# Kernel optimization log

Hardware: AMD Instinct MI355X
Metric: run time of the kernel (lower is better)

## Reference

```python
import jax, jax.numpy as jnp
import numpy as np

N_EMBD = 1024
N_HEAD = 16

def setup_inputs() -> dict:
    key = jax.random.key(0)
    ks = jax.random.split(key, 8)
    C = N_EMBD
    s = 1.0 / np.sqrt(C)
    return {
        "x": jax.random.normal(ks[0], (8, 1024, C), jnp.float32),
        "encoder_output": jax.random.normal(ks[1], (8, 576, C), jnp.float32),
        "Wq": jax.random.normal(ks[2], (C, C), jnp.float32) * s,      # torch Linear weight [out,in]
        "bq": jnp.zeros((C,), jnp.float32),
        "Wkv": jax.random.normal(ks[3], (2 * C, C), jnp.float32) * s,
        "bkv": jnp.zeros((2 * C,), jnp.float32),
        "Wo": jax.random.normal(ks[4], (C, C), jnp.float32) * s,
        "bo": jnp.zeros((C,), jnp.float32),
    }

def reference(x, encoder_output, Wq, bq, Wkv, bkv, Wo, bo):
    B, T, C = x.shape
    I = encoder_output.shape[1]
    H, D = N_HEAD, C // N_HEAD
    q = jnp.einsum('btc,oc->bto', x, Wq) + bq                     # [B,T,C]
    kv = jnp.einsum('bic,oc->bio', encoder_output, Wkv) + bkv     # [B,I,2C]
    k, v = kv[..., :C], kv[..., C:]
    q = q.reshape(B, T, H, D).transpose(0, 2, 1, 3)               # [B,H,T,D]
    k = k.reshape(B, I, H, D).transpose(0, 2, 1, 3)               # [B,H,I,D]
    v = v.reshape(B, I, H, D).transpose(0, 2, 1, 3)               # [B,H,I,D]
    att = jnp.einsum('bhtd,bhid->bhti', q, k) * (1.0 / np.sqrt(D))
    att = jax.nn.softmax(att, axis=-1)                            # no mask: buffer unused in fwd
    y = jnp.einsum('bhti,bhid->bhtd', att, v)
    y = y.transpose(0, 2, 1, 3).reshape(B, T, C)
    return jnp.einsum('btc,oc->bto', y, Wo) + bo
```

## Files before the change

kernel.cpp:

```cpp
#include <hip/hip_runtime.h>
#include <type_traits>

typedef __bf16 bf16_t;
typedef __bf16 bfx8 __attribute__((ext_vector_type(8)));
typedef float  fx4  __attribute__((ext_vector_type(4)));

#define MFMA_BF16 __builtin_amdgcn_mfma_f32_16x16x32_bf16

#define BB 8
#define TT 1024
#define II 576
#define HH 16
#define DD 64
#define CC 1024

__device__ __forceinline__ void load_lds16(const void* g, void* l) {
    __builtin_amdgcn_global_load_lds(
        (const __attribute__((address_space(1))) void*)g,
        (__attribute__((address_space(3))) void*)l, 16, 0, 0);
}

__global__ __launch_bounds__(256)
void cvt_all(const float* __restrict__ x,  const float* __restrict__ enc,
             const float* __restrict__ wq, const float* __restrict__ wkv,
             const float* __restrict__ wo, const float* __restrict__ bq,
             const float* __restrict__ bkv,const float* __restrict__ bo,
             bf16_t* __restrict__ xb,  bf16_t* __restrict__ encb,
             bf16_t* __restrict__ wqb, bf16_t* __restrict__ wkvb,
             bf16_t* __restrict__ wob, bf16_t* __restrict__ bqb,
             bf16_t* __restrict__ bkvb,bf16_t* __restrict__ bob)
{
    const long total = 17305600;
    for (long e = ((long)blockIdx.x * 256 + threadIdx.x) * 8; e < total;
         e += (long)gridDim.x * 256 * 8) {
        const float* s; bf16_t* d; long off; float sc = 1.0f;
        if      (e <  8388608) { s = x;   d = xb;   off = e; }
        else if (e < 13107200) { s = enc; d = encb; off = e -  8388608; }
        else if (e < 14155776) { s = wq;  d = wqb;  off = e - 13107200; sc = 0.125f; }
        else if (e < 16252928) { s = wkv; d = wkvb; off = e - 14155776; }
        else if (e < 17301504) { s = wo;  d = wob;  off = e - 16252928; }
        else if (e < 17302528) { s = bq;  d = bqb;  off = e - 17301504; sc = 0.125f; }
        else if (e < 17304576) { s = bkv; d = bkvb; off = e - 17302528; }
        else                   { s = bo;  d = bob;  off = e - 17304576; }
        fx4 a = *reinterpret_cast<const fx4*>(s + off);
        fx4 b = *reinterpret_cast<const fx4*>(s + off + 4);
        bfx8 v;
#pragma unroll
        for (int i = 0; i < 4; i++) {
            v[i]     = (bf16_t)(a[i] * sc);
            v[4 + i] = (bf16_t)(b[i] * sc);
        }
        *reinterpret_cast<bfx8*>(d + off) = v;
    }
}

template<typename TOUT>
__global__ __launch_bounds__(256)
void gemm_lds(const bf16_t* __restrict__ A, const bf16_t* __restrict__ W,
              const bf16_t* __restrict__ bias, TOUT* __restrict__ out,
              int M, int N, int K)
{
    __shared__ __align__(16) bf16_t As[128 * 64];
    __shared__ __align__(16) bf16_t Bs[128 * 64];

    const int tid  = threadIdx.x;
    const int lane = tid & 63;
    const int w    = tid >> 6;
    const int wm   = (w >> 1) * 64;
    const int wn   = (w & 1) * 64;
    const int m0   = blockIdx.y * 128;
    const int n0   = blockIdx.x * 128;
    const int lrow = lane & 15;
    const int quad = lane >> 4;

    fx4 acc[4][4];
#pragma unroll
    for (int i = 0; i < 4; i++)
#pragma unroll
        for (int j = 0; j < 4; j++) acc[i][j] = (fx4)0.0f;

    for (int k0 = 0; k0 < K; k0 += 64) {
        __syncthreads();
#pragma unroll
        for (int j = 0; j < 4; j++) {
            int e0  = (w * 4 + j) * 512;
            int e   = e0 + lane * 8;
            int row = e >> 6;
            int col = e & 63;
            load_lds16(&A[(long)(m0 + row) * K + k0 + col], &As[e0]);
            load_lds16(&W[(long)(n0 + row) * K + k0 + col], &Bs[e0]);
        }
        __syncthreads();

#pragma unroll
        for (int kk = 0; kk < 2; kk++) {
            bfx8 af[4], bfr[4];
#pragma unroll
            for (int i = 0; i < 4; i++)
                af[i] = *reinterpret_cast<const bfx8*>(
                    &As[(wm + i * 16 + lrow) * 64 + kk * 32 + quad * 8]);
#pragma unroll
            for (int j = 0; j < 4; j++)
                bfr[j] = *reinterpret_cast<const bfx8*>(
                    &Bs[(wn + j * 16 + lrow) * 64 + kk * 32 + quad * 8]);
#pragma unroll
            for (int i = 0; i < 4; i++)
#pragma unroll
                for (int j = 0; j < 4; j++)
                    acc[i][j] = MFMA_BF16(af[i], bfr[j], acc[i][j], 0, 0, 0);
        }
    }

#pragma unroll
    for (int i = 0; i < 4; i++) {
#pragma unroll
        for (int j = 0; j < 4; j++) {
            int col  = n0 + wn + j * 16 + lrow;
            float bv = (float)bias[col];
            int row0 = m0 + wm + i * 16 + quad * 4;
#pragma unroll
            for (int r = 0; r < 4; r++)
                out[(long)(row0 + r) * N + col] = (TOUT)(acc[i][j][r] + bv);
        }
    }
}

template<typename TA, typename TOUT>
__global__ __launch_bounds__(256)
void gemm_bt_bias(const TA* __restrict__ A, const float* __restrict__ W,
                  const float* __restrict__ bias, TOUT* __restrict__ out,
                  int M, int N, int K, float escale)
{
    __shared__ __align__(16) bf16_t As[128][40];
    __shared__ __align__(16) bf16_t Bs[128][40];

    const int tid  = threadIdx.x;
    const int lane = tid & 63;
    const int wave = tid >> 6;
    const int wm   = (wave >> 1) * 64;
    const int wn   = (wave & 1) * 64;
    const int m0   = blockIdx.y * 128;
    const int n0   = blockIdx.x * 128;
    const int lrow = lane & 15;
    const int quad = lane >> 4;

    fx4 acc[4][4];
#pragma unroll
    for (int i = 0; i < 4; i++)
#pragma unroll
        for (int j = 0; j < 4; j++) acc[i][j] = (fx4)0.0f;

    for (int k0 = 0; k0 < K; k0 += 32) {
        __syncthreads();
#pragma unroll
        for (int r = 0; r < 2; ++r) {
            int idx = tid + r * 256;
            int row = idx >> 2;
            int col = (idx & 3) * 8;

            bfx8 av;
            if constexpr (std::is_same<TA, float>::value) {
                const float* sa = &A[(long)(m0 + row) * K + k0 + col];
                fx4 a0 = *reinterpret_cast<const fx4*>(sa);
                fx4 a1 = *reinterpret_cast<const fx4*>(sa + 4);
#pragma unroll
                for (int e = 0; e < 4; e++) {
                    av[e]     = (bf16_t)a0[e];
                    av[4 + e] = (bf16_t)a1[e];
                }
            } else {
                av = *reinterpret_cast<const bfx8*>(&A[(long)(m0 + row) * K + k0 + col]);
            }
            *reinterpret_cast<bfx8*>(&As[row][col]) = av;

            const float* sw = &W[(long)(n0 + row) * K + k0 + col];
            fx4 b0 = *reinterpret_cast<const fx4*>(sw);
            fx4 b1 = *reinterpret_cast<const fx4*>(sw + 4);
            bfx8 bv;
#pragma unroll
            for (int e = 0; e < 4; e++) {
                bv[e]     = (bf16_t)b0[e];
                bv[4 + e] = (bf16_t)b1[e];
            }
            *reinterpret_cast<bfx8*>(&Bs[row][col]) = bv;
        }
        __syncthreads();

        bfx8 af[4], bfr[4];
#pragma unroll
        for (int i = 0; i < 4; i++)
            af[i] = *reinterpret_cast<const bfx8*>(&As[wm + i * 16 + lrow][quad * 8]);
#pragma unroll
        for (int j = 0; j < 4; j++)
            bfr[j] = *reinterpret_cast<const bfx8*>(&Bs[wn + j * 16 + lrow][quad * 8]);
#pragma unroll
        for (int i = 0; i < 4; i++)
#pragma unroll
            for (int j = 0; j < 4; j++)
                acc[i][j] = MFMA_BF16(af[i], bfr[j], acc[i][j], 0, 0, 0);
    }

#pragma unroll
    for (int i = 0; i < 4; i++) {
#pragma unroll
        for (int j = 0; j < 4; j++) {
            int col  = n0 + wn + j * 16 + lrow;
            float bv = bias[col];
            int row0 = m0 + wm + i * 16 + quad * 4;
#pragma unroll
            for (int r = 0; r < 4; r++)
                out[(long)(row0 + r) * N + col] = (TOUT)((acc[i][j][r] + bv) * escale);
        }
    }
}

__global__ __launch_bounds__(256)
void attn_kernel(const bf16_t* __restrict__ q, const bf16_t* __restrict__ kv,
                 bf16_t* __restrict__ y, int b0)
{
    __shared__ __align__(16) bf16_t Ks[64][72];
    __shared__ __align__(16) bf16_t Vt[64][72];
    __shared__ __align__(16) bf16_t Ps[4][16][72];

    const int tid  = threadIdx.x;
    const int lane = tid & 63;
    const int w    = tid >> 6;
    const int lrow = lane & 15;
    const int quad = lane >> 4;
    const int bl = blockIdx.z;
    const int b  = b0 + bl;
    const int h  = blockIdx.y;
    const int t0 = blockIdx.x * 64;

    const int trow = t0 + w * 16 + lrow;
    bfx8 qf[2];
#pragma unroll
    for (int ks = 0; ks < 2; ++ks)
        qf[ks] = *reinterpret_cast<const bfx8*>(
            &q[(long)(b * TT + trow) * CC + h * 64 + ks * 32 + quad * 8]);

    float mrow[4], lsum[4];
    fx4 o[4];
#pragma unroll
    for (int r = 0; r < 4; r++) { mrow[r] = -1e30f; lsum[r] = 0.f; }
#pragma unroll
    for (int dt = 0; dt < 4; dt++) o[dt] = (fx4)0.0f;

    const int srow = tid >> 2;
    const int scol = (tid & 3) * 16;

    for (int ic = 0; ic < II / 64; ++ic) {
        __syncthreads();
        {
            long base = (long)(bl * II + ic * 64 + srow) * 2048 + h * 64 + scol;
            bfx8 k0v = *reinterpret_cast<const bfx8*>(&kv[base]);
            bfx8 k1v = *reinterpret_cast<const bfx8*>(&kv[base + 8]);
            *reinterpret_cast<bfx8*>(&Ks[srow][scol])     = k0v;
            *reinterpret_cast<bfx8*>(&Ks[srow][scol + 8]) = k1v;
            bfx8 v0 = *reinterpret_cast<const bfx8*>(&kv[base + 1024]);
            bfx8 v1 = *reinterpret_cast<const bfx8*>(&kv[base + 1032]);
#pragma unroll
            for (int e = 0; e < 8; e++) {
                Vt[scol + e][srow]     = v0[e];
                Vt[scol + 8 + e][srow] = v1[e];
            }
        }
        __syncthreads();

        fx4 s[4];
#pragma unroll
        for (int nt = 0; nt < 4; nt++) {
            s[nt] = (fx4)0.0f;
#pragma unroll
            for (int ks = 0; ks < 2; ks++) {
                bfx8 bf = *reinterpret_cast<const bfx8*>(
                    &Ks[nt * 16 + lrow][ks * 32 + quad * 8]);
                s[nt] = MFMA_BF16(qf[ks], bf, s[nt], 0, 0, 0);
            }
        }

        float p[4][4];
#pragma unroll
        for (int r = 0; r < 4; r++) {
            float mx = -1e30f;
#pragma unroll
            for (int nt = 0; nt < 4; nt++) mx = fmaxf(mx, s[nt][r]);
#pragma unroll
            for (int off = 1; off < 16; off <<= 1)
                mx = fmaxf(mx, __shfl_xor(mx, off, 64));
            float mnew  = fmaxf(mrow[r], mx);
            float alpha = __expf(mrow[r] - mnew);
            mrow[r] = mnew;
            float ps = 0.f;
#pragma unroll
            for (int nt = 0; nt < 4; nt++) {
                float pv = __expf(s[nt][r] - mnew);
                p[nt][r] = pv;
                ps += pv;
            }
#pragma unroll
            for (int off = 1; off < 16; off <<= 1)
                ps += __shfl_xor(ps, off, 64);
            lsum[r] = lsum[r] * alpha + ps;
#pragma unroll
            for (int dt = 0; dt < 4; dt++) o[dt][r] *= alpha;
        }

#pragma unroll
        for (int nt = 0; nt < 4; nt++)
#pragma unroll
            for (int r = 0; r < 4; r++)
                Ps[w][quad * 4 + r][nt * 16 + lrow] = (bf16_t)p[nt][r];

        __asm__ __volatile__("s_waitcnt lgkmcnt(0)" ::: "memory");

#pragma unroll
        for (int dt = 0; dt < 4; dt++) {
#pragma unroll
            for (int ks = 0; ks < 2; ks++) {
                bfx8 af = *reinterpret_cast<const bfx8*>(
                    &Ps[w][lrow][ks * 32 + quad * 8]);
                bfx8 bf = *reinterpret_cast<const bfx8*>(
                    &Vt[dt * 16 + lrow][ks * 32 + quad * 8]);
                o[dt] = MFMA_BF16(af, bf, o[dt], 0, 0, 0);
            }
        }
    }

#pragma unroll
    for (int dt = 0; dt < 4; dt++) {
#pragma unroll
        for (int r = 0; r < 4; r++) {
            int t = t0 + w * 16 + quad * 4 + r;
            y[(long)(b * TT + t) * CC + h * 64 + dt * 16 + lrow] =
                (bf16_t)(o[dt][r] / lsum[r]);
        }
    }
}

extern "C" void kernel_launch(void* const* d_in, const int* in_sizes, int n_in,
                              void* d_out, int out_size, void* d_ws, size_t ws_size,
                              hipStream_t stream)
{
    const float* x   = (const float*)d_in[0];
    const float* enc = (const float*)d_in[1];
    const float* Wq  = (const float*)d_in[2];
    const float* bq  = (const float*)d_in[3];
    const float* Wkv = (const float*)d_in[4];
    const float* bkv = (const float*)d_in[5];
    const float* Wo  = (const float*)d_in[6];
    const float* bo  = (const float*)d_in[7];
    float* out = (float*)d_out;

    bf16_t* qbuf = (bf16_t*)d_out;

    const size_t primary_need = 35520512ULL * 2;

    if (ws_size >= primary_need) {
        bf16_t* kvbuf = (bf16_t*)d_ws;
        bf16_t* ybuf  = kvbuf + (size_t)9437184;
        bf16_t* xb    = ybuf  + (size_t)8388608;
        bf16_t* encb  = xb    + (size_t)8388608;
        bf16_t* Wqb   = encb  + (size_t)4718592;
        bf16_t* Wkvb  = Wqb   + (size_t)1048576;
        bf16_t* Wob   = Wkvb  + (size_t)2097152;
        bf16_t* bqb   = Wob   + (size_t)1048576;
        bf16_t* bkvb  = bqb   + 1024;
        bf16_t* bob   = bkvb  + 2048;

        cvt_all<<<4096, 256, 0, stream>>>(x, enc, Wq, Wkv, Wo, bq, bkv, bo,
                                          xb, encb, Wqb, Wkvb, Wob, bqb, bkvb, bob);

        gemm_lds<bf16_t><<<dim3(8, 64), 256, 0, stream>>>(
            xb, Wqb, bqb, qbuf, 8192, 1024, 1024);
        gemm_lds<bf16_t><<<dim3(16, 36), 256, 0, stream>>>(
            encb, Wkvb, bkvb, kvbuf, 4608, 2048, 1024);
        attn_kernel<<<dim3(16, 16, 8), 256, 0, stream>>>(qbuf, kvbuf, ybuf, 0);
        gemm_lds<float><<<dim3(8, 64), 256, 0, stream>>>(
            ybuf, Wob, bob, out, 8192, 1024, 1024);
    } else {
        bf16_t* kvbuf = (bf16_t*)d_ws;
        gemm_bt_bias<float, bf16_t><<<dim3(8, 64), 256, 0, stream>>>(
            x, Wq, bq, qbuf, 8192, 1024, 1024, 0.125f);

        const size_t full_need = ((size_t)4608 * 2048 + (size_t)8192 * 1024) * 2;
        if (ws_size >= full_need) {
            bf16_t* ybuf = kvbuf + (size_t)4608 * 2048;
            gemm_bt_bias<float, bf16_t><<<dim3(16, 36), 256, 0, stream>>>(
                enc, Wkv, bkv, kvbuf, 4608, 2048, 1024, 1.0f);
            attn_kernel<<<dim3(16, 16, 8), 256, 0, stream>>>(qbuf, kvbuf, ybuf, 0);
            gemm_bt_bias<bf16_t, float><<<dim3(8, 64), 256, 0, stream>>>(
                ybuf, Wo, bo, out, 8192, 1024, 1024, 1.0f);
        } else {
            bf16_t* ybuf = kvbuf + (size_t)1152 * 2048;
            for (int b0 = 0; b0 < BB; b0 += 2) {
                gemm_bt_bias<float, bf16_t><<<dim3(16, 9), 256, 0, stream>>>(
                    enc + (size_t)b0 * II * CC, Wkv, bkv, kvbuf, 1152, 2048, 1024, 1.0f);
                attn_kernel<<<dim3(16, 16, 2), 256, 0, stream>>>(qbuf, kvbuf, ybuf, b0);
            }
            gemm_bt_bias<bf16_t, float><<<dim3(8, 64), 256, 0, stream>>>(
                ybuf, Wo, bo, out, 8192, 1024, 1024, 1.0f);
        }
    }
}
```

Measured before the change: 297.7 us.

## Fuse Q and KV projections, swizzle LDS, pre-layout K/V^T for attention

Merges the Q and KV projection GEMMs into one launch and shrinks the GEMM tile to 128x64 so more blocks are in flight. An XOR swizzle on the LDS column index is meant to cut bank conflicts. The KV epilogue writes K as head-major and V already transposed, so attention can load tiles with plain vector copies. The new attention kernel gives each wave 32 query rows to reuse K/V tiles, and drops the max subtraction from the softmax. The cost is strided, uncoalesced scatter stores in the KV epilogue and an unguarded exp that could overflow on larger scores.

```diff
diff --git a/kernel.cpp b/kernel.cpp
--- a/kernel.cpp
+++ b/kernel.cpp
@@ -54,67 +54,183 @@
     }
 }
 
-template<typename TOUT>
+
+#define GEMM_STAGE(A_, W_, K_)                                                \
+    {                                                                         \
+        _Pragma("unroll")                                                     \
+        for (int j = 0; j < 4; j++) {                                         \
+            int e0  = (w * 4 + j) * 512;                                      \
+            int row = (e0 >> 6) + (lane >> 3);                                \
+            load_lds16(&A_[(long)(m0 + row) * K_ + k0 + colsw], &As[e0]);     \
+        }                                                                     \
+        _Pragma("unroll")                                                     \
+        for (int j = 0; j < 2; j++) {                                         \
+            int e0  = (w * 2 + j) * 512;                                      \
+            int row = (e0 >> 6) + (lane >> 3);                                \
+            load_lds16(&W_[(long)(n0 + row) * K_ + k0 + colsw], &Bs[e0]);     \
+        }                                                                     \
+    }
+
+#define GEMM_MFMA()                                                           \
+    _Pragma("unroll")                                                         \
+    for (int kk = 0; kk < 2; kk++) {                                          \
+        bfx8 af[4], bfr[2];                                                   \
+        _Pragma("unroll")                                                     \
+        for (int i = 0; i < 4; i++) {                                         \
+            int R = wm + i * 16 + lrow;                                       \
+            af[i] = *reinterpret_cast<const bfx8*>(                           \
+                &As[R * 64 + (((kk * 4 + quad) ^ (lrow & 7)) * 8)]);          \
+        }                                                                     \
+        _Pragma("unroll")                                                     \
+        for (int j = 0; j < 2; j++) {                                         \
+            int R = wn + j * 16 + lrow;                                       \
+            bfr[j] = *reinterpret_cast<const bfx8*>(                          \
+                &Bs[R * 64 + (((kk * 4 + quad) ^ (lrow & 7)) * 8)]);          \
+        }                                                                     \
+        _Pragma("unroll")                                                     \
+        for (int i = 0; i < 4; i++)                                           \
+            _Pragma("unroll")                                                 \
+            for (int j = 0; j < 2; j++)                                       \
+                acc[i][j] = MFMA_BF16(af[i], bfr[j], acc[i][j], 0, 0, 0);     \
+    }
+
 __global__ __launch_bounds__(256)
-void gemm_lds(const bf16_t* __restrict__ A, const bf16_t* __restrict__ W,
-              const bf16_t* __restrict__ bias, TOUT* __restrict__ out,
-              int M, int N, int K)
+void gemm_qkv(const bf16_t* __restrict__ xb,  const bf16_t* __restrict__ Wqb,
+              const bf16_t* __restrict__ bqb, bf16_t* __restrict__ qout,
+              const bf16_t* __restrict__ encb,const bf16_t* __restrict__ Wkvb,
+              const bf16_t* __restrict__ bkvb,
+              bf16_t* __restrict__ Kbuf, bf16_t* __restrict__ VTbuf)
 {
     __shared__ __align__(16) bf16_t As[128 * 64];
-    __shared__ __align__(16) bf16_t Bs[128 * 64];
+    __shared__ __align__(16) bf16_t Bs[64 * 64];
 
     const int tid  = threadIdx.x;
     const int lane = tid & 63;
     const int w    = tid >> 6;
     const int wm   = (w >> 1) * 64;
-    const int wn   = (w & 1) * 64;
-    const int m0   = blockIdx.y * 128;
-    const int n0   = blockIdx.x * 128;
+    const int wn   = (w & 1) * 32;
     const int lrow = lane & 15;
     const int quad = lane >> 4;
-
-    fx4 acc[4][4];
+    const int colsw = (((lane & 7) ^ ((lane >> 3) & 7)) * 8);
+
+    int bid = blockIdx.x;
+    const bf16_t *A, *W, *bias;
+    int m0, n0, mode;
+    if (bid < 1024) {
+        mode = 0; A = xb; W = Wqb; bias = bqb;
+        m0 = (bid >> 4) * 128; n0 = (bid & 15) * 64;
+    } else {
+        bid -= 1024;
+        mode = 1; A = encb; W = Wkvb; bias = bkvb;
+        m0 = (bid >> 5) * 128; n0 = (bid & 31) * 64;
+    }
+    const int K = 1024;
+
+    fx4 acc[4][2];
 #pragma unroll
     for (int i = 0; i < 4; i++)
 #pragma unroll
-        for (int j = 0; j < 4; j++) acc[i][j] = (fx4)0.0f;
+        for (int j = 0; j < 2; j++) acc[i][j] = (fx4)0.0f;
 
     for (int k0 = 0; k0 < K; k0 += 64) {
         __syncthreads();
-#pragma unroll
-        for (int j = 0; j < 4; j++) {
-            int e0  = (w * 4 + j) * 512;
-            int e   = e0 + lane * 8;
-            int row = e >> 6;
-            int col = e & 63;
-            load_lds16(&A[(long)(m0 + row) * K + k0 + col], &As[e0]);
-            load_lds16(&W[(long)(n0 + row) * K + k0 + col], &Bs[e0]);
-        }
-        __syncthreads();
-
-#pragma unroll
-        for (int kk = 0; kk < 2; kk++) {
-            bfx8 af[4], bfr[4];
-#pragma unroll
-            for (int i = 0; i < 4; i++)
-                af[i] = *reinterpret_cast<const bfx8*>(
-                    &As[(wm + i * 16 + lrow) * 64 + kk * 32 + quad * 8]);
-#pragma unroll
-            for (int j = 0; j < 4; j++)
-                bfr[j] = *reinterpret_cast<const bfx8*>(
-                    &Bs[(wn + j * 16 + lrow) * 64 + kk * 32 + quad * 8]);
-#pragma unroll
-            for (int i = 0; i < 4; i++)
-#pragma unroll
-                for (int j = 0; j < 4; j++)
-                    acc[i][j] = MFMA_BF16(af[i], bfr[j], acc[i][j], 0, 0, 0);
-        }
-    }
-
-#pragma unroll
-    for (int i = 0; i < 4; i++) {
-#pragma unroll
-        for (int j = 0; j < 4; j++) {
+        GEMM_STAGE(A, W, K)
+        __syncthreads();
+        GEMM_MFMA()
+    }
+
+    if (mode == 0) {
+#pragma unroll
+        for (int i = 0; i < 4; i++)
+#pragma unroll
+            for (int j = 0; j < 2; j++) {
+                int col  = n0 + wn + j * 16 + lrow;
+                float bv = (float)bias[col];
+                int row0 = m0 + wm + i * 16 + quad * 4;
+#pragma unroll
+                for (int r = 0; r < 4; r++)
+                    qout[(long)(row0 + r) * 1024 + col] =
+                        (bf16_t)(acc[i][j][r] + bv);
+            }
+    } else if (n0 < 1024) {
+#pragma unroll
+        for (int i = 0; i < 4; i++) {
+            int row0 = m0 + wm + i * 16 + quad * 4;
+#pragma unroll
+            for (int r = 0; r < 4; r++) {
+                unsigned m = row0 + r;
+                unsigned b = m / 576u;
+                unsigned ii = m - b * 576u;
+#pragma unroll
+                for (int j = 0; j < 2; j++) {
+                    int col = n0 + wn + j * 16 + lrow;
+                    int h = col >> 6, d = col & 63;
+                    Kbuf[(((long)(b * 16 + h) * 576 + ii) << 6) + d] =
+                        (bf16_t)(acc[i][j][r] + (float)bias[col]);
+                }
+            }
+        }
+    } else {
+#pragma unroll
+        for (int i = 0; i < 4; i++) {
+            int row0 = m0 + wm + i * 16 + quad * 4;
+#pragma unroll
+            for (int r = 0; r < 4; r++) {
+                unsigned m = row0 + r;
+                unsigned b = m / 576u;
+                unsigned ii = m - b * 576u;
+#pragma unroll
+                for (int j = 0; j < 2; j++) {
+                    int col = n0 + wn + j * 16 + lrow;
+                    int c2 = col - 1024;
+                    int h = c2 >> 6, d = c2 & 63;
+                    VTbuf[((long)(b * 16 + h) * 64 + d) * 576 + ii] =
+                        (bf16_t)(acc[i][j][r] + (float)bias[col]);
+                }
+            }
+        }
+    }
+}
+
+template<typename TOUT>
+__global__ __launch_bounds__(256)
+void gemm2(const bf16_t* __restrict__ A, const bf16_t* __restrict__ W,
+           const bf16_t* __restrict__ bias, TOUT* __restrict__ out,
+           int M, int N, int K)
+{
+    __shared__ __align__(16) bf16_t As[128 * 64];
+    __shared__ __align__(16) bf16_t Bs[64 * 64];
+
+    const int tid  = threadIdx.x;
+    const int lane = tid & 63;
+    const int w    = tid >> 6;
+    const int wm   = (w >> 1) * 64;
+    const int wn   = (w & 1) * 32;
+    const int lrow = lane & 15;
+    const int quad = lane >> 4;
+    const int colsw = (((lane & 7) ^ ((lane >> 3) & 7)) * 8);
+
+    const int ntiles = N >> 6;
+    const int m0 = (blockIdx.x / ntiles) * 128;
+    const int n0 = (blockIdx.x % ntiles) * 64;
+
+    fx4 acc[4][2];
+#pragma unroll
+    for (int i = 0; i < 4; i++)
+#pragma unroll
+        for (int j = 0; j < 2; j++) acc[i][j] = (fx4)0.0f;
+
+    for (int k0 = 0; k0 < K; k0 += 64) {
+        __syncthreads();
+        GEMM_STAGE(A, W, K)
+        __syncthreads();
+        GEMM_MFMA()
+    }
+
+#pragma unroll
+    for (int i = 0; i < 4; i++)
+#pragma unroll
+        for (int j = 0; j < 2; j++) {
             int col  = n0 + wn + j * 16 + lrow;
             float bv = (float)bias[col];
             int row0 = m0 + wm + i * 16 + quad * 4;
@@ -122,7 +238,117 @@
             for (int r = 0; r < 4; r++)
                 out[(long)(row0 + r) * N + col] = (TOUT)(acc[i][j][r] + bv);
         }
-    }
+}
+
+__global__ __launch_bounds__(256)
+void attn2(const bf16_t* __restrict__ q, const bf16_t* __restrict__ Kbuf,
+           const bf16_t* __restrict__ VTbuf, bf16_t* __restrict__ y)
+{
+    __shared__ __align__(16) bf16_t Ks[64][72];
+    __shared__ __align__(16) bf16_t Vt[64][72];
+    __shared__ __align__(16) bf16_t Ps[4][32][72];
+
+    const int tid  = threadIdx.x;
+    const int lane = tid & 63;
+    const int w    = tid >> 6;
+    const int lrow = lane & 15;
+    const int quad = lane >> 4;
+    const int b  = blockIdx.z;
+    const int h  = blockIdx.y;
+    const int t0 = blockIdx.x * 128;
+
+    const bf16_t* kb = Kbuf  + ((long)(b * 16 + h) * 576) * 64;
+    const bf16_t* vb = VTbuf + ((long)(b * 16 + h) * 64) * 576;
+
+    bfx8 qf[2][2];
+#pragma unroll
+    for (int mt = 0; mt < 2; mt++)
+#pragma unroll
+        for (int ks = 0; ks < 2; ks++)
+            qf[mt][ks] = *reinterpret_cast<const bfx8*>(
+                &q[(long)(b * TT + t0 + w * 32 + mt * 16 + lrow) * CC +
+                   h * 64 + ks * 32 + quad * 8]);
+
+    fx4 o[2][4];
+    float lsum[2][4];
+#pragma unroll
+    for (int mt = 0; mt < 2; mt++)
+#pragma unroll
+        for (int dt = 0; dt < 4; dt++) o[mt][dt] = (fx4)0.0f;
+#pragma unroll
+    for (int mt = 0; mt < 2; mt++)
+#pragma unroll
+        for (int r = 0; r < 4; r++) lsum[mt][r] = 0.f;
+
+    const int srow = tid >> 3;
+    const int scol = (tid & 7) * 8;
+
+    for (int ic = 0; ic < II / 64; ++ic) {
+        __syncthreads();
+#pragma unroll
+        for (int it = 0; it < 2; it++) {
+            int rr = srow + it * 32;
+            *reinterpret_cast<bfx8*>(&Ks[rr][scol]) =
+                *reinterpret_cast<const bfx8*>(&kb[(long)(ic * 64 + rr) * 64 + scol]);
+            *reinterpret_cast<bfx8*>(&Vt[rr][scol]) =
+                *reinterpret_cast<const bfx8*>(&vb[(long)rr * 576 + ic * 64 + scol]);
+        }
+        __syncthreads();
+
+#pragma unroll
+        for (int mt = 0; mt < 2; mt++) {
+            fx4 s[4];
+#pragma unroll
+            for (int nt = 0; nt < 4; nt++) {
+                s[nt] = (fx4)0.0f;
+#pragma unroll
+                for (int ks = 0; ks < 2; ks++) {
+                    bfx8 bfr = *reinterpret_cast<const bfx8*>(
+                        &Ks[nt * 16 + lrow][ks * 32 + quad * 8]);
+                    s[nt] = MFMA_BF16(qf[mt][ks], bfr, s[nt], 0, 0, 0);
+                }
+            }
+#pragma unroll
+            for (int nt = 0; nt < 4; nt++)
+#pragma unroll
+                for (int r = 0; r < 4; r++) {
+                    float p = __expf(s[nt][r]);
+                    lsum[mt][r] += p;
+                    Ps[w][mt * 16 + quad * 4 + r][nt * 16 + lrow] = (bf16_t)p;
+                }
+        }
+
+        __asm__ __volatile__("s_waitcnt lgkmcnt(0)" ::: "memory");
+
+#pragma unroll
+        for (int mt = 0; mt < 2; mt++)
+#pragma unroll
+            for (int dt = 0; dt < 4; dt++)
+#pragma unroll
+                for (int ks = 0; ks < 2; ks++) {
+                    bfx8 af = *reinterpret_cast<const bfx8*>(
+                        &Ps[w][mt * 16 + lrow][ks * 32 + quad * 8]);
+                    bfx8 bfr = *reinterpret_cast<const bfx8*>(
+                        &Vt[dt * 16 + lrow][ks * 32 + quad * 8]);
+                    o[mt][dt] = MFMA_BF16(af, bfr, o[mt][dt], 0, 0, 0);
+                }
+    }
+
+#pragma unroll
+    for (int mt = 0; mt < 2; mt++)
+#pragma unroll
+        for (int r = 0; r < 4; r++) {
+            float l = lsum[mt][r];
+#pragma unroll
+            for (int off = 1; off < 16; off <<= 1)
+                l += __shfl_xor(l, off, 64);
+            float inv = 1.0f / l;
+            int t = t0 + w * 32 + mt * 16 + quad * 4 + r;
+#pragma unroll
+            for (int dt = 0; dt < 4; dt++)
+                y[(long)(b * TT + t) * CC + h * 64 + dt * 16 + lrow] =
+                    (bf16_t)(o[mt][dt][r] * inv);
+        }
 }
 
 template<typename TA, typename TOUT>
@@ -157,31 +383,23 @@
             int idx = tid + r * 256;
             int row = idx >> 2;
             int col = (idx & 3) * 8;
-
             bfx8 av;
             if constexpr (std::is_same<TA, float>::value) {
                 const float* sa = &A[(long)(m0 + row) * K + k0 + col];
                 fx4 a0 = *reinterpret_cast<const fx4*>(sa);
                 fx4 a1 = *reinterpret_cast<const fx4*>(sa + 4);
 #pragma unroll
-                for (int e = 0; e < 4; e++) {
-                    av[e]     = (bf16_t)a0[e];
-                    av[4 + e] = (bf16_t)a1[e];
-                }
+                for (int e = 0; e < 4; e++) { av[e] = (bf16_t)a0[e]; av[4+e] = (bf16_t)a1[e]; }
             } else {
                 av = *reinterpret_cast<const bfx8*>(&A[(long)(m0 + row) * K + k0 + col]);
             }
             *reinterpret_cast<bfx8*>(&As[row][col]) = av;
-
             const float* sw = &W[(long)(n0 + row) * K + k0 + col];
             fx4 b0 = *reinterpret_cast<const fx4*>(sw);
             fx4 b1 = *reinterpret_cast<const fx4*>(sw + 4);
             bfx8 bv;
 #pragma unroll
-            for (int e = 0; e < 4; e++) {
-                bv[e]     = (bf16_t)b0[e];
-                bv[4 + e] = (bf16_t)b1[e];
-            }
+            for (int e = 0; e < 4; e++) { bv[e] = (bf16_t)b0[e]; bv[4+e] = (bf16_t)b1[e]; }
             *reinterpret_cast<bfx8*>(&Bs[row][col]) = bv;
         }
         __syncthreads();
@@ -201,7 +419,7 @@
     }
 
 #pragma unroll
-    for (int i = 0; i < 4; i++) {
+    for (int i = 0; i < 4; i++)
 #pragma unroll
         for (int j = 0; j < 4; j++) {
             int col  = n0 + wn + j * 16 + lrow;
@@ -211,7 +429,6 @@
             for (int r = 0; r < 4; r++)
                 out[(long)(row0 + r) * N + col] = (TOUT)((acc[i][j][r] + bv) * escale);
         }
-    }
 }
 
 __global__ __launch_bounds__(256)
@@ -273,9 +490,9 @@
             s[nt] = (fx4)0.0f;
 #pragma unroll
             for (int ks = 0; ks < 2; ks++) {
-                bfx8 bf = *reinterpret_cast<const bfx8*>(
+                bfx8 bfr = *reinterpret_cast<const bfx8*>(
                     &Ks[nt * 16 + lrow][ks * 32 + quad * 8]);
-                s[nt] = MFMA_BF16(qf[ks], bf, s[nt], 0, 0, 0);
+                s[nt] = MFMA_BF16(qf[ks], bfr, s[nt], 0, 0, 0);
             }
         }
 
@@ -315,27 +532,25 @@
         __asm__ __volatile__("s_waitcnt lgkmcnt(0)" ::: "memory");
 
 #pragma unroll
-        for (int dt = 0; dt < 4; dt++) {
+        for (int dt = 0; dt < 4; dt++)
 #pragma unroll
             for (int ks = 0; ks < 2; ks++) {
                 bfx8 af = *reinterpret_cast<const bfx8*>(
                     &Ps[w][lrow][ks * 32 + quad * 8]);
-                bfx8 bf = *reinterpret_cast<const bfx8*>(
+                bfx8 bfr = *reinterpret_cast<const bfx8*>(
                     &Vt[dt * 16 + lrow][ks * 32 + quad * 8]);
-                o[dt] = MFMA_BF16(af, bf, o[dt], 0, 0, 0);
-            }
-        }
-    }
-
-#pragma unroll
-    for (int dt = 0; dt < 4; dt++) {
+                o[dt] = MFMA_BF16(af, bfr, o[dt], 0, 0, 0);
+            }
+    }
+
+#pragma unroll
+    for (int dt = 0; dt < 4; dt++)
 #pragma unroll
         for (int r = 0; r < 4; r++) {
             int t = t0 + w * 16 + quad * 4 + r;
             y[(long)(b * TT + t) * CC + h * 64 + dt * 16 + lrow] =
                 (bf16_t)(o[dt][r] / lsum[r]);
         }
-    }
 }
 
 extern "C" void kernel_launch(void* const* d_in, const int* in_sizes, int n_in,
@@ -354,11 +569,12 @@
 
     bf16_t* qbuf = (bf16_t*)d_out;
 
-    const size_t primary_need = 35520512ULL * 2;
+    const size_t primary_need = 35131392ULL * 2;
 
     if (ws_size >= primary_need) {
-        bf16_t* kvbuf = (bf16_t*)d_ws;
-        bf16_t* ybuf  = kvbuf + (size_t)9437184;
+        bf16_t* Kbuf  = (bf16_t*)d_ws;
+        bf16_t* VTbuf = Kbuf  + (size_t)4718592;
+        bf16_t* ybuf  = VTbuf + (size_t)4718592;
         bf16_t* xb    = ybuf  + (size_t)8388608;
         bf16_t* encb  = xb    + (size_t)8388608;
         bf16_t* Wqb   = encb  + (size_t)4718592;
@@ -370,19 +586,15 @@
 
         cvt_all<<<4096, 256, 0, stream>>>(x, enc, Wq, Wkv, Wo, bq, bkv, bo,
                                           xb, encb, Wqb, Wkvb, Wob, bqb, bkvb, bob);
-
-        gemm_lds<bf16_t><<<dim3(8, 64), 256, 0, stream>>>(
-            xb, Wqb, bqb, qbuf, 8192, 1024, 1024);
-        gemm_lds<bf16_t><<<dim3(16, 36), 256, 0, stream>>>(
-            encb, Wkvb, bkvb, kvbuf, 4608, 2048, 1024);
-        attn_kernel<<<dim3(16, 16, 8), 256, 0, stream>>>(qbuf, kvbuf, ybuf, 0);
-        gemm_lds<float><<<dim3(8, 64), 256, 0, stream>>>(
-            ybuf, Wob, bob, out, 8192, 1024, 1024);
+        gemm_qkv<<<2176, 256, 0, stream>>>(xb, Wqb, bqb, qbuf,
+                                           encb, Wkvb, bkvb, Kbuf, VTbuf);
+        attn2<<<dim3(8, 16, 8), 256, 0, stream>>>(qbuf, Kbuf, VTbuf, ybuf);
+        gemm2<float><<<1024, 256, 0, stream>>>(ybuf, Wob, bob, out,
+                                               8192, 1024, 1024);
     } else {
         bf16_t* kvbuf = (bf16_t*)d_ws;
         gemm_bt_bias<float, bf16_t><<<dim3(8, 64), 256, 0, stream>>>(
             x, Wq, bq, qbuf, 8192, 1024, 1024, 0.125f);
-
         const size_t full_need = ((size_t)4608 * 2048 + (size_t)8192 * 1024) * 2;
         if (ws_size >= full_need) {
             bf16_t* ybuf = kvbuf + (size_t)4608 * 2048;
```

Measured after the change: 241.3 us. 19.0% less time.
